# Optimization experiments

Measured on AMD Instinct MI355X. Metric: run time of the kernel, lower is better.

Reference implementation:

```python
import jax, jax.numpy as jnp
import numpy as np

DIM = 2048      # model dim
H = 32          # num_heads
N = 128         # state_dim
G = 1           # num_groups
K = 4           # conv_size
HID = 4096     # hidden_dim = multiple_of*ceil(2.0*DIM/256)
P = HID // H    # head_dim = 128
CHUNK = 256
EPS = 1e-6
DT_MIN, DT_MAX = 0.001, 0.1


def setup_inputs() -> dict:
    key = jax.random.key(0)
    ks = jax.random.split(key, 8)
    b, s = 2, 2048
    d_in = 2 * HID + 2 * G * N + H           # 8448
    conv_dim = HID + 2 * G * N               # 4352
    return {
        "x": jax.random.normal(ks[0], (b, s, DIM), jnp.float32),
        "W_in": jax.random.normal(ks[1], (d_in, DIM), jnp.float32) / np.sqrt(DIM),
        "conv_w": jax.random.normal(ks[2], (conv_dim, K), jnp.float32) / np.sqrt(K),
        "conv_b": jnp.zeros((conv_dim,), jnp.float32),
        "dt_bias": jnp.zeros((H,), jnp.float32),
        "A_log": jnp.log(jax.random.uniform(ks[3], (H,), jnp.float32, 1.0, 16.0)),
        "D": jnp.ones((H,), jnp.float32),
        "norm_w": jnp.ones((HID,), jnp.float32),
        "W_out": jax.random.normal(ks[4], (DIM, HID), jnp.float32) / np.sqrt(HID),
    }


def _causal_conv_silu(xBC, w, bias):
    # depthwise causal conv1d, kernel K, then SiLU. xBC: (b,s,c), w: (c,K)
    b, s, c = xBC.shape
    xp = jnp.pad(xBC, ((0, 0), (K - 1, 0), (0, 0)))
    y = sum(xp[:, k:k + s, :] * w[:, k] for k in range(K)) + bias
    return jax.nn.silu(y)


def _chunked_scan(x, dt, A, B, C, D):
    # Mamba2 chunked selective scan.
    # x:(b,s,h,p) dt:(b,s,h) A:(h,) B,C:(b,s,n) (groups=1) D:(h,)
    b, s, h, p = x.shape
    n = B.shape[-1]
    nc, L = s // CHUNK, CHUNK
    xc = x.reshape(b, nc, L, h, p)
    dtc = dt.reshape(b, nc, L, h)
    Bc = B.reshape(b, nc, L, n)
    Cc = C.reshape(b, nc, L, n)

    dA = dtc * A                          # (b,nc,L,h), A<0
    dA_cs = jnp.cumsum(dA, axis=2)        # (b,nc,L,h)

    # intra-chunk contribution
    seg = dA_cs[:, :, :, None, :] - dA_cs[:, :, None, :, :]   # (b,nc,L,L,h)
    mask = jnp.tril(jnp.ones((L, L), bool))[None, None, :, :, None]
    decay = jnp.exp(jnp.where(mask, seg, -jnp.inf))
    CB = jnp.einsum('bcln,bcsn->bcls', Cc, Bc)                # (b,nc,L,L)
    y_intra = jnp.einsum('bcls,bclsh,bcsh,bcshp->bclhp', CB, decay, dtc, xc)

    # per-chunk final states
    decay_states = jnp.exp(dA_cs[:, :, -1:, :] - dA_cs)       # (b,nc,L,h)
    states = jnp.einsum('bclh,bclh,bclhp,bcln->bchpn', decay_states, dtc, xc, Bc)

    # inter-chunk recurrence over chunk index
    dA_chunk = dA_cs[:, :, -1, :]                              # (b,nc,h)
    def step(prev, inp):
        st, dec = inp
        new = prev * jnp.exp(dec)[:, :, None, None] + st
        return new, prev
    init = jnp.zeros((b, h, p, n), x.dtype)
    _, prev_states = jax.lax.scan(step, init,
                                  (jnp.moveaxis(states, 1, 0), jnp.moveaxis(dA_chunk, 1, 0)))
    prev_states = jnp.moveaxis(prev_states, 0, 1)              # state at start of each chunk

    y_inter = jnp.einsum('bcln,bclh,bchpn->bclhp', Cc, jnp.exp(dA_cs), prev_states)
    y = (y_intra + y_inter).reshape(b, s, h, p)
    return y + x * D[None, None, :, None]


def reference(x, W_in, conv_w, conv_b, dt_bias, A_log, D, norm_w, W_out):
    b, s, _ = x.shape
    zxbcdt = x @ W_in.T                                        # (b,s,2*HID+2GN+H)
    z, xBC, dt = jnp.split(zxbcdt, [HID, 2 * HID + 2 * G * N], axis=-1)
    xBC = _causal_conv_silu(xBC, conv_w, conv_b)
    xs, B, C = jnp.split(xBC, [HID, HID + G * N], axis=-1)
    A = -jnp.exp(A_log)
    dt = jnp.clip(jax.nn.softplus(dt + dt_bias), DT_MIN, DT_MAX)
    xs = xs.reshape(b, s, H, P)
    y = _chunked_scan(xs, dt, A, B, C, D).reshape(b, s, HID)
    y = y * jax.nn.silu(z)                                     # gate, norm_before_gate=False
    y = y * jax.lax.rsqrt(jnp.mean(y * y, axis=-1, keepdims=True) + EPS) * norm_w
    return y @ W_out.T
```

## Files before the change

kernel.cpp:

```cpp
#include <hip/hip_runtime.h>


typedef short s16x8 __attribute__((ext_vector_type(8)));
typedef float f32x4 __attribute__((ext_vector_type(4)));

__device__ __forceinline__ float bf2f(ushort u) {
    return __builtin_bit_cast(float, (unsigned)u << 16);
}
__device__ __forceinline__ ushort f2bf(float f) {
    unsigned u = __builtin_bit_cast(unsigned, f);
    unsigned r = u + 0x7fffu + ((u >> 16) & 1u);
    return (ushort)(r >> 16);
}

__device__ __forceinline__ void gld16(const void* g, void* l) {
    __builtin_amdgcn_global_load_lds((__attribute__((address_space(1))) void*)g,
                                     (__attribute__((address_space(3))) void*)l, 16, 0, 0);
}

#define BARRIER() asm volatile("s_barrier" ::: "memory")

__global__ void cast_all_k(const float4* __restrict__ x, const float4* __restrict__ wout,
                           const float4* __restrict__ win, ushort* __restrict__ xb,
                           ushort* __restrict__ woutb, ushort* __restrict__ winb) {
    const long b = blockIdx.x, tid = threadIdx.x;
    if (b < 8192) {
        long i = b * 256 + tid;
        float4 v = x[i];
        ushort4 o = { f2bf(v.x), f2bf(v.y), f2bf(v.z), f2bf(v.w) };
        *(ushort4*)(xb + i * 4) = o;
    } else if (b < 16384) {
        long i = (b - 8192) * 256 + tid;
        float4 v = wout[i];
        ushort4 o = { f2bf(v.x), f2bf(v.y), f2bf(v.z), f2bf(v.w) };
        *(ushort4*)(woutb + i * 4) = o;
    } else {
        long i = (b - 16384) * 256 + tid;
        ushort4 o;
        if (i < 4341760L) {
            float4 v = win[i];
            o = { f2bf(v.x), f2bf(v.y), f2bf(v.z), f2bf(v.w) };
        } else {
            o = { 0, 0, 0, 0 };
        }
        *(ushort4*)(winb + i * 4) = o;
    }
}

__global__ __launch_bounds__(512, 1) void gemm1_k(const ushort* __restrict__ A,
                                                  const ushort* __restrict__ Bm,
                                                  ushort* __restrict__ zbuf,
                                                  ushort* __restrict__ xbc,
                                                  ushort* __restrict__ dtr) {
    constexpr int K = 2048, NT = 64;
    __shared__ ushort lds[3 * 8192 + 3 * 6144];
    const int tid = threadIdx.x, lane = tid & 63, wave = tid >> 6;
    const int wm = wave >> 2, wn = wave & 3;
    const int bid = blockIdx.x;
    const int xcd = bid & 7, w = bid >> 3;
    const int mt = xcd * 2 + (w & 1), nt = w >> 1;
    const long m0 = (long)mt * 256, n0 = (long)nt * 192;

    const int st_row = lane >> 2;
    const int st_gc = ((lane & 3) * 8) ^ (((lane >> 5) & 1) << 4);

    auto STAGE_A = [&](int buf, int kt) {
#pragma unroll
        for (int j = 0; j < 2; j++) {
            int sidx = wave + j * 8;
            gld16(A + (m0 + sidx * 16 + st_row) * K + kt + st_gc,
                  lds + buf * 8192 + sidx * 512 + lane * 8);
        }
    };
    auto STAGE_B = [&](int buf, int kt) {
#pragma unroll
        for (int j = 0; j < 2; j++) {
            int sidx = wave + j * 8;
            if (sidx < 12)
                gld16(Bm + (n0 + sidx * 16 + st_row) * K + kt + st_gc,
                      lds + 24576 + buf * 6144 + sidx * 512 + lane * 8);
        }
    };

    const int cfr = (lane >> 4) * 8;
    const int lr = lane & 15;
    auto LDFA = [&](int buf, int r) -> s16x8 {
        int off = buf * 8192 + ((r >> 4) << 9) + ((r & 15) << 5)
                + (cfr ^ (((r >> 3) & 1) << 4));
        return *(const s16x8*)(lds + off);
    };
    auto LDFB = [&](int buf, int r) -> s16x8 {
        int off = 24576 + buf * 6144 + ((r >> 4) << 9) + ((r & 15) << 5)
                + (cfr ^ (((r >> 3) & 1) << 4));
        return *(const s16x8*)(lds + off);
    };

    f32x4 zero = { 0.f, 0.f, 0.f, 0.f };
    f32x4 acc[8][3];
#pragma unroll
    for (int i = 0; i < 8; i++)
#pragma unroll
        for (int j = 0; j < 3; j++) acc[i][j] = zero;

    STAGE_A(0, 0);  STAGE_B(0, 0);
    STAGE_A(1, 32); STAGE_B(1, 32);
    asm volatile("s_waitcnt vmcnt(3)" ::: "memory");
    BARRIER();

    for (int t = 0; t < NT; ++t) {
        const int cur = t % 3;
        const int nxt = (t + 2) % 3;
        const int kt2 = (t + 2) * 32;
        const bool do_stage = (t + 2) < NT;

        s16x8 bfr[3], afr[4];
#pragma unroll
        for (int ni = 0; ni < 3; ni++) bfr[ni] = LDFB(cur, wn * 48 + ni * 16 + lr);
#pragma unroll
        for (int mi = 0; mi < 4; mi++) afr[mi] = LDFA(cur, wm * 128 + mi * 16 + lr);
        if (do_stage) STAGE_A(nxt, kt2);
        BARRIER();
        __builtin_amdgcn_s_setprio(1);
#pragma unroll
        for (int mi = 0; mi < 4; mi++)
#pragma unroll
            for (int ni = 0; ni < 3; ni++)
                acc[mi][ni] = __builtin_amdgcn_mfma_f32_16x16x32_bf16(afr[mi], bfr[ni], acc[mi][ni], 0, 0, 0);
        __builtin_amdgcn_s_setprio(0);
        BARRIER();

#pragma unroll
        for (int mi = 0; mi < 4; mi++) afr[mi] = LDFA(cur, wm * 128 + 64 + mi * 16 + lr);
        if (do_stage) STAGE_B(nxt, kt2);
        BARRIER();
        __builtin_amdgcn_s_setprio(1);
#pragma unroll
        for (int mi = 0; mi < 4; mi++)
#pragma unroll
            for (int ni = 0; ni < 3; ni++)
                acc[mi + 4][ni] = __builtin_amdgcn_mfma_f32_16x16x32_bf16(afr[mi], bfr[ni], acc[mi + 4][ni], 0, 0, 0);
        __builtin_amdgcn_s_setprio(0);
        asm volatile("s_waitcnt vmcnt(3)" ::: "memory");
        BARRIER();
    }

    const int lr4 = (lane >> 4) * 4;
#pragma unroll
    for (int mi = 0; mi < 8; mi++) {
#pragma unroll
        for (int ni = 0; ni < 3; ni++) {
            const long col = n0 + wn * 48 + ni * 16 + lr;
            ushort* dst;
            long stride;
            if (col < 4096)      { dst = zbuf + col;         stride = 4096; }
            else if (col < 8448) { dst = xbc + (col - 4096); stride = 4352; }
            else if (col < 8480) { dst = dtr + (col - 8448); stride = 32;   }
            else continue;
            const long row0 = m0 + wm * 128 + mi * 16 + lr4;
#pragma unroll
            for (int r = 0; r < 4; r++) dst[(row0 + r) * stride] = f2bf(acc[mi][ni][r]);
        }
    }
}

__global__ __launch_bounds__(256) void gemm_bt_k(const ushort* __restrict__ A,
                                                 const ushort* __restrict__ Bm,
                                                 float* __restrict__ Cout,
                                                 int Ncols, int Kd) {
    __shared__ ushort As[128 * 32];
    __shared__ ushort Bs[128 * 32];
    const int bid = blockIdx.x;
    const int xcd = bid & 7, w = bid >> 3;
    const int mt = xcd * 4 + (w & 3), nt = w >> 2;
    const int tid = threadIdx.x;
    const int lane = tid & 63, wave = tid >> 6;
    const int wm = wave >> 1, wn = wave & 1;
    const long m0 = (long)mt * 128, n0 = (long)nt * 128;

    f32x4 zero = { 0.f, 0.f, 0.f, 0.f };
    f32x4 acc[4][4];
#pragma unroll
    for (int i = 0; i < 4; i++)
#pragma unroll
        for (int j = 0; j < 4; j++) acc[i][j] = zero;

    const int eb = wave * 512 + lane * 8;
    for (int kt = 0; kt < Kd; kt += 32) {
        __syncthreads();
#pragma unroll
        for (int j = 0; j < 2; j++) {
            int e = j * 2048 + eb;
            int row = e >> 5, col = e & 31;
            gld16(A + (m0 + row) * Kd + kt + col, As + e);
            gld16(Bm + (n0 + row) * Kd + kt + col, Bs + e);
        }
        asm volatile("s_waitcnt vmcnt(0)" ::: "memory");
        __syncthreads();
        s16x8 af[4], bfr[4];
        const int ra = (wm * 64 + (lane & 15)) * 32 + (lane >> 4) * 8;
        const int rb = (wn * 64 + (lane & 15)) * 32 + (lane >> 4) * 8;
#pragma unroll
        for (int i = 0; i < 4; i++) {
            af[i] = *(const s16x8*)(As + ra + i * 512);
            bfr[i] = *(const s16x8*)(Bs + rb + i * 512);
        }
#pragma unroll
        for (int mi = 0; mi < 4; mi++)
#pragma unroll
            for (int ni = 0; ni < 4; ni++)
                acc[mi][ni] = __builtin_amdgcn_mfma_f32_16x16x32_bf16(af[mi], bfr[ni], acc[mi][ni], 0, 0, 0);
    }
    const long crow = m0 + wm * 64 + ((lane >> 4) << 2);
    const long ccol = n0 + wn * 64 + (lane & 15);
#pragma unroll
    for (int mi = 0; mi < 4; mi++)
#pragma unroll
        for (int ni = 0; ni < 4; ni++)
#pragma unroll
            for (int r = 0; r < 4; r++)
                Cout[(crow + mi * 16 + r) * (long)Ncols + ccol + ni * 16] = acc[mi][ni][r];
}

__global__ __launch_bounds__(256) void convx_k(const ushort* __restrict__ xbc,
                                               const float* __restrict__ w,
                                               const float* __restrict__ bias,
                                               ushort* __restrict__ xbcc,
                                               ushort* __restrict__ xT,
                                               ushort* __restrict__ Bt) {
    __shared__ ushort xin[35][136];
    __shared__ ushort yL[32][132];
    const int stile = blockIdx.x, slot = blockIdx.y, bc = blockIdx.z;
    const int tid = threadIdx.x;
    const int cc = bc & 7;
    const long tbase = (long)bc * 256 + stile * 32;
    const int c0 = slot * 128;
    const bool head = (cc == 0 && stile == 0);

#pragma unroll
    for (int i = 0; i < 3; i++) {
        int u = tid + i * 256;
        if (u < 560) {
            int r = u >> 4, seg = u & 15;
            s16x8 v;
            if (head && r < 3) {
#pragma unroll
                for (int j = 0; j < 8; j++) v[j] = 0;
            } else {
                v = *(const s16x8*)&xbc[(tbase - 3 + r) * 4352 + c0 + seg * 8];
            }
            *(s16x8*)&xin[r][seg * 8] = v;
        }
    }
    __syncthreads();

    const int s_loc = tid >> 3, p0 = (tid & 7) * 16;
    ushort yo[16];
#pragma unroll
    for (int j = 0; j < 16; j++) {
        int c = p0 + j;
        float a = bias[c0 + c];
#pragma unroll
        for (int k = 0; k < 4; k++)
            a += bf2f(xin[s_loc + k][c]) * w[(c0 + c) * 4 + k];
        float yv = a / (1.f + __expf(-a));
        ushort ub = f2bf(yv);
        yo[j] = ub;
        yL[s_loc][c] = ub;
    }
    *(s16x8*)&xbcc[(tbase + s_loc) * 4352 + c0 + p0] = *(const s16x8*)&yo[0];
    *(s16x8*)&xbcc[(tbase + s_loc) * 4352 + c0 + p0 + 8] = *(const s16x8*)&yo[8];
    __syncthreads();

    if (slot < 33) {
        const int p = tid >> 1, s0 = (tid & 1) * 16;
        ushort o[16];
#pragma unroll
        for (int j = 0; j < 16; j++) o[j] = yL[s0 + j][p];
        ushort* dst = (slot < 32)
            ? (xT + ((long)(bc * 32 + slot) * 128 + p) * 256 + stile * 32 + s0)
            : (Bt + ((long)bc * 128 + p) * 256 + stile * 32 + s0);
        *(s16x8*)&dst[0] = *(const s16x8*)&o[0];
        *(s16x8*)&dst[8] = *(const s16x8*)&o[8];
    }
}

__global__ void prep_k(const ushort* __restrict__ dtr, const float* __restrict__ dt_bias,
                       const float* __restrict__ A_log, float* __restrict__ dtp,
                       float* __restrict__ dacs) {
    const int bx = blockIdx.x;
    const int h = bx & 31, cc = (bx >> 5) & 7, bi = bx >> 8;
    const int lane = threadIdx.x;
    const float A = -__expf(A_log[h]);
    const float bsh = dt_bias[h];
    float v[4], cs[4];
    float run = 0.f;
#pragma unroll
    for (int j = 0; j < 4; j++) {
        int pos = cc * 256 + lane * 4 + j;
        float raw = bf2f(dtr[((long)(bi * 2048 + pos)) * 32 + h]) + bsh;
        float sp = (raw > 20.f) ? raw : log1pf(__expf(raw));
        float d = fminf(fmaxf(sp, 0.001f), 0.1f);
        v[j] = d;
        run += d * A;
        cs[j] = run;
    }
    float tot = run, pre = run;
    for (int off = 1; off < 64; off <<= 1) {
        float u = __shfl_up(pre, off, 64);
        if (lane >= off) pre += u;
    }
    float excl = pre - tot;
    const long base = ((long)(bi * 32 + h)) * 2048 + cc * 256 + lane * 4;
#pragma unroll
    for (int j = 0; j < 4; j++) { dtp[base + j] = v[j]; dacs[base + j] = excl + cs[j]; }
}

__global__ __launch_bounds__(256) void cb_mfma_k(const ushort* __restrict__ xbcc,
                                                 float* __restrict__ CB) {
    const int bid = blockIdx.x;
    const int sq = bid & 1, lq = (bid >> 1) & 1, bc = bid >> 2;
    const int tid = threadIdx.x, lane = tid & 63, wave = tid >> 6;
    const int wm = wave >> 1, wn = wave & 1;
    const long tbase = (long)bc * 256;

    f32x4 zero = { 0.f, 0.f, 0.f, 0.f };
    f32x4 acc[4][4];
#pragma unroll
    for (int i = 0; i < 4; i++)
#pragma unroll
        for (int j = 0; j < 4; j++) acc[i][j] = zero;

    for (int kst = 0; kst < 4; ++kst) {
        const int koff = kst * 32 + (lane >> 4) * 8;
        s16x8 a[4], b[4];
#pragma unroll
        for (int mi = 0; mi < 4; mi++) {
            int l = lq * 128 + wm * 64 + mi * 16 + (lane & 15);
            a[mi] = *(const s16x8*)&xbcc[(tbase + l) * 4352 + 4224 + koff];
        }
#pragma unroll
        for (int ni = 0; ni < 4; ni++) {
            int s = sq * 128 + wn * 64 + ni * 16 + (lane & 15);
            b[ni] = *(const s16x8*)&xbcc[(tbase + s) * 4352 + 4096 + koff];
        }
#pragma unroll
        for (int mi = 0; mi < 4; mi++)
#pragma unroll
            for (int ni = 0; ni < 4; ni++)
                acc[mi][ni] = __builtin_amdgcn_mfma_f32_16x16x32_bf16(a[mi], b[ni], acc[mi][ni], 0, 0, 0);
    }

    float* out = CB + (long)bc * 65536;
#pragma unroll
    for (int mi = 0; mi < 4; mi++)
#pragma unroll
        for (int ni = 0; ni < 4; ni++)
#pragma unroll
            for (int r = 0; r < 4; r++) {
                int l = lq * 128 + wm * 64 + mi * 16 + (lane >> 4) * 4 + r;
                int s = sq * 128 + wn * 64 + ni * 16 + (lane & 15);
                out[(long)l * 256 + s] = acc[mi][ni][r];
            }
}

__global__ __launch_bounds__(256) void intra_mfma_k(const ushort* __restrict__ xT,
                                                    const float* __restrict__ CB,
                                                    const float* __restrict__ dtp,
                                                    const float* __restrict__ dacs,
                                                    float* __restrict__ yf) {
    const int bx = blockIdx.x;
    const int ltile = bx & 1, h = (bx >> 1) & 31, cc = (bx >> 6) & 7, bi = bx >> 9;
    const int tid = threadIdx.x, lane = tid & 63, wave = tid >> 6;
    const int wm = wave >> 1, wn = wave & 1;

    __shared__ float dA_s[256];
    __shared__ float F_s[256];

    const long dbase = ((long)(bi * 32 + h)) * 2048 + cc * 256;
    {
        float a = dacs[dbase + tid];
        float r = dacs[dbase + (tid | 31)];
        dA_s[tid] = a;
        F_s[tid] = __expf(r - a) * dtp[dbase + tid];
    }
    __syncthreads();

    int lch[4];
    float dAl[4];
#pragma unroll
    for (int mi = 0; mi < 4; mi++) {
        lch[mi] = ltile * 128 + wm * 64 + mi * 16 + (lane & 15);
        dAl[mi] = dA_s[lch[mi]];
    }

    f32x4 zero = { 0.f, 0.f, 0.f, 0.f };
    f32x4 acc[4][4];
#pragma unroll
    for (int i = 0; i < 4; i++)
#pragma unroll
        for (int j = 0; j < 4; j++) acc[i][j] = zero;

    const long tbase = (long)bi * 2048 + cc * 256;
    const long cbbase = ((long)(bi * 8 + cc)) * 65536;
    const ushort* xrow = xT + (((long)(bi * 8 + cc) * 32 + h) * 128) * 256;
    const int nsb = ltile * 4 + 4;

    for (int sb = 0; sb < nsb; ++sb) {
        const int soff = sb * 32 + (lane >> 4) * 8;
        s16x8 bf[4];
#pragma unroll
        for (int ni = 0; ni < 4; ni++) {
            int p = wn * 64 + ni * 16 + (lane & 15);
            bf[ni] = *(const s16x8*)&xrow[(long)p * 256 + soff];
        }
        const float Rsb = dA_s[sb * 32 + 31];
        const int s0 = soff;
#pragma unroll
        for (int mi = 0; mi < 4; mi++) {
            const int lb = lch[mi] >> 5;
            if (sb > lb) continue;
            const float* cbrow = CB + cbbase + (long)lch[mi] * 256 + s0;
            float4 c0 = *(const float4*)cbrow;
            float4 c1 = *(const float4*)(cbrow + 4);
            float E = __expf(dAl[mi] - Rsb);
            float m[8];
            m[0] = c0.x * E * F_s[s0 + 0]; m[1] = c0.y * E * F_s[s0 + 1];
            m[2] = c0.z * E * F_s[s0 + 2]; m[3] = c0.w * E * F_s[s0 + 3];
            m[4] = c1.x * E * F_s[s0 + 4]; m[5] = c1.y * E * F_s[s0 + 5];
            m[6] = c1.z * E * F_s[s0 + 6]; m[7] = c1.w * E * F_s[s0 + 7];
            if (sb == lb) {
#pragma unroll
                for (int j = 0; j < 8; j++)
                    if (s0 + j > lch[mi]) m[j] = 0.f;
            }
            s16x8 a;
#pragma unroll
            for (int j = 0; j < 8; j++) a[j] = (short)f2bf(m[j]);
#pragma unroll
            for (int ni = 0; ni < 4; ni++)
                acc[mi][ni] = __builtin_amdgcn_mfma_f32_16x16x32_bf16(a, bf[ni], acc[mi][ni], 0, 0, 0);
        }
    }

    const long crow = tbase + ltile * 128 + wm * 64 + ((lane >> 4) << 2);
    const int ccol = h * 128 + wn * 64 + (lane & 15);
#pragma unroll
    for (int mi = 0; mi < 4; mi++)
#pragma unroll
        for (int ni = 0; ni < 4; ni++)
#pragma unroll
            for (int r = 0; r < 4; r++)
                yf[(crow + mi * 16 + r) * 4096 + ccol + ni * 16] = acc[mi][ni][r];
}

__global__ __launch_bounds__(256) void states_mfma_k(const ushort* __restrict__ xT,
                                                     const ushort* __restrict__ Bt,
                                                     const float* __restrict__ dtp,
                                                     const float* __restrict__ dacs,
                                                     float* __restrict__ states) {
    const int bx = blockIdx.x;
    const int h = bx & 31, cc = (bx >> 5) & 7, bi = bx >> 8;
    const int bc = bi * 8 + cc;
    const int tid = threadIdx.x, lane = tid & 63, wave = tid >> 6;
    const int wm = wave >> 1, wn = wave & 1;
    __shared__ float wl[256];
    const long dbase = ((long)(bi * 32 + h)) * 2048 + cc * 256;
    {
        float last = dacs[dbase + 255];
        wl[tid] = __expf(last - dacs[dbase + tid]) * dtp[dbase + tid];
    }
    __syncthreads();

    f32x4 zero = { 0.f, 0.f, 0.f, 0.f };
    f32x4 acc[4][4];
#pragma unroll
    for (int i = 0; i < 4; i++)
#pragma unroll
        for (int j = 0; j < 4; j++) acc[i][j] = zero;

    const ushort* xrow = xT + (((long)bc * 32 + h) * 128) * 256;
    const ushort* brow = Bt + ((long)bc * 128) * 256;

    for (int sb = 0; sb < 8; ++sb) {
        const int soff = sb * 32 + (lane >> 4) * 8;
        s16x8 a[4], b[4];
#pragma unroll
        for (int mi = 0; mi < 4; mi++) {
            int p = wm * 64 + mi * 16 + (lane & 15);
            s16x8 raw = *(const s16x8*)&xrow[(long)p * 256 + soff];
#pragma unroll
            for (int j = 0; j < 8; j++)
                a[mi][j] = (short)f2bf(bf2f((ushort)raw[j]) * wl[soff + j]);
        }
#pragma unroll
        for (int ni = 0; ni < 4; ni++) {
            int n = wn * 64 + ni * 16 + (lane & 15);
            b[ni] = *(const s16x8*)&brow[(long)n * 256 + soff];
        }
#pragma unroll
        for (int mi = 0; mi < 4; mi++)
#pragma unroll
            for (int ni = 0; ni < 4; ni++)
                acc[mi][ni] = __builtin_amdgcn_mfma_f32_16x16x32_bf16(a[mi], b[ni], acc[mi][ni], 0, 0, 0);
    }

    float* out = states + (((long)bc * 32 + h) * 128) * 128;
#pragma unroll
    for (int mi = 0; mi < 4; mi++)
#pragma unroll
        for (int ni = 0; ni < 4; ni++)
#pragma unroll
            for (int r = 0; r < 4; r++) {
                int p = wm * 64 + mi * 16 + (lane >> 4) * 4 + r;
                int n = wn * 64 + ni * 16 + (lane & 15);
                out[(long)p * 128 + n] = acc[mi][ni][r];
            }
}

__global__ void rec_k(float* __restrict__ states, const float* __restrict__ dacs) {
    const int i = blockIdx.x * 256 + threadIdx.x;
    const int n = i & 127, p = (i >> 7) & 127, h = (i >> 14) & 31, bi = i >> 19;
    const long dbase = ((long)(bi * 32 + h)) * 2048;
    float run = 0.f;
    for (int cc = 0; cc < 8; cc++) {
        const long off = ((((long)(bi * 8 + cc)) * 32 + h) * 128 + p) * 128 + n;
        float st = states[off];
        states[off] = run;
        float dec = dacs[dbase + cc * 256 + 255];
        run = run * __expf(dec) + st;
    }
}

__global__ __launch_bounds__(256) void inter_mfma_k(const ushort* __restrict__ xbcc,
                                                    const float* __restrict__ st,
                                                    const float* __restrict__ dacs,
                                                    float* __restrict__ yf) {
    const int bx = blockIdx.x;
    const int lt = bx & 1, h = (bx >> 1) & 31, cc = (bx >> 6) & 7, bi = bx >> 9;
    const int tid = threadIdx.x, lane = tid & 63, wave = tid >> 6;
    const int wm = wave >> 1, wn = wave & 1;
    __shared__ float eA[256];
    const long dbase = ((long)(bi * 32 + h)) * 2048 + cc * 256;
    eA[tid] = __expf(dacs[dbase + tid]);
    __syncthreads();

    const long tbase = (long)bi * 2048 + cc * 256;
    const float* sbase = st + (((long)(bi * 8 + cc) * 32 + h) * 128) * 128;

    f32x4 zero = { 0.f, 0.f, 0.f, 0.f };
    f32x4 acc[4][4];
#pragma unroll
    for (int i = 0; i < 4; i++)
#pragma unroll
        for (int j = 0; j < 4; j++) acc[i][j] = zero;

    for (int kk = 0; kk < 4; ++kk) {
        const int koff = kk * 32 + (lane >> 4) * 8;
        s16x8 a[4], b[4];
#pragma unroll
        for (int mi = 0; mi < 4; mi++) {
            int l = lt * 128 + wm * 64 + mi * 16 + (lane & 15);
            a[mi] = *(const s16x8*)&xbcc[(tbase + l) * 4352 + 4224 + koff];
        }
#pragma unroll
        for (int ni = 0; ni < 4; ni++) {
            int p = wn * 64 + ni * 16 + (lane & 15);
            const float* pr = sbase + (long)p * 128 + koff;
            float4 v0 = *(const float4*)pr;
            float4 v1 = *(const float4*)(pr + 4);
            b[ni][0] = (short)f2bf(v0.x); b[ni][1] = (short)f2bf(v0.y);
            b[ni][2] = (short)f2bf(v0.z); b[ni][3] = (short)f2bf(v0.w);
            b[ni][4] = (short)f2bf(v1.x); b[ni][5] = (short)f2bf(v1.y);
            b[ni][6] = (short)f2bf(v1.z); b[ni][7] = (short)f2bf(v1.w);
        }
#pragma unroll
        for (int mi = 0; mi < 4; mi++)
#pragma unroll
            for (int ni = 0; ni < 4; ni++)
                acc[mi][ni] = __builtin_amdgcn_mfma_f32_16x16x32_bf16(a[mi], b[ni], acc[mi][ni], 0, 0, 0);
    }

#pragma unroll
    for (int mi = 0; mi < 4; mi++)
#pragma unroll
        for (int r = 0; r < 4; r++) {
            int l = lt * 128 + wm * 64 + mi * 16 + (lane >> 4) * 4 + r;
            float e = eA[l];
            float* yr = &yf[(tbase + l) * 4096 + h * 128];
#pragma unroll
            for (int ni = 0; ni < 4; ni++) {
                int p = wn * 64 + ni * 16 + (lane & 15);
                yr[p] += e * acc[mi][ni][r];
            }
        }
}

__global__ __launch_bounds__(256) void gate_rms_k(const float* __restrict__ y, const ushort* __restrict__ zbuf,
                                                  const ushort* __restrict__ xbcc, const float* __restrict__ Dv,
                                                  const float* __restrict__ norm_w, ushort* __restrict__ yb) {
    const int t = blockIdx.x, tid = threadIdx.x;
    const float* yr = &y[(long)t * 4096];
    const ushort* zr = &zbuf[(long)t * 4096];
    const ushort* xr = &xbcc[(long)t * 4352];
    float g[16];
    float ss = 0.f;
#pragma unroll
    for (int j = 0; j < 16; j++) {
        int i = j * 256 + tid;
        float z = bf2f(zr[i]);
        float yv = yr[i] + Dv[i >> 7] * bf2f(xr[i]);
        float gv = yv * (z / (1.f + __expf(-z)));
        g[j] = gv;
        ss += gv * gv;
    }
#pragma unroll
    for (int off = 32; off > 0; off >>= 1) ss += __shfl_xor(ss, off, 64);
    __shared__ float red[4];
    if ((tid & 63) == 0) red[tid >> 6] = ss;
    __syncthreads();
    float tot = red[0] + red[1] + red[2] + red[3];
    float sc = rsqrtf(tot * (1.f / 4096.f) + 1e-6f);
#pragma unroll
    for (int j = 0; j < 16; j++) {
        int i = j * 256 + tid;
        yb[(long)t * 4096 + i] = f2bf(g[j] * sc * norm_w[i]);
    }
}

extern "C" void kernel_launch(void* const* d_in, const int* in_sizes, int n_in,
                              void* d_out, int out_size, void* d_ws, size_t ws_size,
                              hipStream_t stream) {
    const float* x       = (const float*)d_in[0];
    const float* W_in    = (const float*)d_in[1];
    const float* conv_w  = (const float*)d_in[2];
    const float* conv_b  = (const float*)d_in[3];
    const float* dt_bias = (const float*)d_in[4];
    const float* A_log   = (const float*)d_in[5];
    const float* Dv      = (const float*)d_in[6];
    const float* norm_w  = (const float*)d_in[7];
    const float* W_out   = (const float*)d_in[8];

    char* w8 = (char*)d_ws;
    ushort* xb    = (ushort*)(w8 + 0L);
    ushort* xT    = (ushort*)(w8 + 0L);
    ushort* yb    = (ushort*)(w8 + 0L);
    ushort* woutb = (ushort*)(w8 + 33554432L);
    ushort* Bt    = (ushort*)(w8 + 50331648L);
    ushort* zbuf  = (ushort*)(w8 + 52428800L);
    ushort* xbc   = (ushort*)(w8 + 85983232L);
    ushort* dtr   = (ushort*)(w8 + 121634816L);
    ushort* xbcc  = (ushort*)(w8 + 121896960L);
    float*  dtp   = (float*)(w8 + 157548544L);
    float*  dacs  = (float*)(w8 + 158072832L);
    float*  cb    = (float*)(w8 + 158597120L);
    float*  yf    = (float*)(w8 + 162791424L);
    ushort* winb  = (ushort*)(w8 + 162791424L);
    float*  st    = (float*)(w8 + 229900288L);

    cast_all_k<<<34048, 256, 0, stream>>>((const float4*)x, (const float4*)W_out,
                                          (const float4*)W_in, xb, woutb, winb);
    gemm1_k<<<736, 512, 0, stream>>>(xb, winb, zbuf, xbc, dtr);
    convx_k<<<dim3(8, 34, 16), 256, 0, stream>>>(xbc, conv_w, conv_b, xbcc, xT, Bt);
    prep_k<<<512, 64, 0, stream>>>(dtr, dt_bias, A_log, dtp, dacs);
    cb_mfma_k<<<64, 256, 0, stream>>>(xbcc, cb);
    intra_mfma_k<<<1024, 256, 0, stream>>>(xT, cb, dtp, dacs, yf);
    states_mfma_k<<<512, 256, 0, stream>>>(xT, Bt, dtp, dacs, st);
    rec_k<<<4096, 256, 0, stream>>>(st, dacs);
    inter_mfma_k<<<1024, 256, 0, stream>>>(xbcc, st, dacs, yf);
    gate_rms_k<<<4096, 256, 0, stream>>>(yf, zbuf, xbcc, Dv, norm_w, yb);
    gemm_bt_k<<<512, 256, 0, stream>>>(yb, woutb, (float*)d_out, 2048, 4096);
}
```

Measured before the change: 502.3 us.

## Fuse intra and inter chunk scan kernels; pipeline output GEMM with triple buffering

The intra-chunk and inter-chunk kernels are merged into one scan kernel. It adds the C·state contribution, with C pre-scaled by exp(dA_cs), into the same accumulators before the single write of yf. This removes one kernel launch and a read-modify-write pass over the fp32 y buffer. The output projection GEMM is replaced by a 256x128-tile, 512-thread kernel with a three-stage LDS pipeline, XOR-swizzled LDS layout and setprio around the MFMAs, aiming to overlap loads with compute. The C pre-scaling rounds to bf16 after multiplying, which slightly changes numerics.

```diff
diff --git a/kernel.cpp b/kernel.cpp
--- a/kernel.cpp
+++ b/kernel.cpp
@@ -163,62 +163,109 @@
     }
 }
 
-__global__ __launch_bounds__(256) void gemm_bt_k(const ushort* __restrict__ A,
-                                                 const ushort* __restrict__ Bm,
-                                                 float* __restrict__ Cout,
-                                                 int Ncols, int Kd) {
-    __shared__ ushort As[128 * 32];
-    __shared__ ushort Bs[128 * 32];
+__global__ __launch_bounds__(512, 1) void gemm2_k(const ushort* __restrict__ A,
+                                                  const ushort* __restrict__ Bm,
+                                                  float* __restrict__ Cout) {
+    constexpr int K = 4096, NT = 128;
+    __shared__ ushort lds[3 * 8192 + 3 * 4096];
+    const int tid = threadIdx.x, lane = tid & 63, wave = tid >> 6;
+    const int wm = wave >> 2, wn = wave & 3;
     const int bid = blockIdx.x;
     const int xcd = bid & 7, w = bid >> 3;
-    const int mt = xcd * 4 + (w & 3), nt = w >> 2;
-    const int tid = threadIdx.x;
-    const int lane = tid & 63, wave = tid >> 6;
-    const int wm = wave >> 1, wn = wave & 1;
-    const long m0 = (long)mt * 128, n0 = (long)nt * 128;
+    const int mt = xcd * 2 + (w & 1), nt = w >> 1;
+    const long m0 = (long)mt * 256, n0 = (long)nt * 128;
+
+    const int st_row = lane >> 2;
+    const int st_gc = ((lane & 3) * 8) ^ (((lane >> 5) & 1) << 4);
+
+    auto STAGE_A = [&](int buf, int kt) {
+#pragma unroll
+        for (int j = 0; j < 2; j++) {
+            int sidx = wave + j * 8;
+            gld16(A + (m0 + sidx * 16 + st_row) * K + kt + st_gc,
+                  lds + buf * 8192 + sidx * 512 + lane * 8);
+        }
+    };
+    auto STAGE_B = [&](int buf, int kt) {
+        int sidx = wave;
+        gld16(Bm + (n0 + sidx * 16 + st_row) * K + kt + st_gc,
+              lds + 24576 + buf * 4096 + sidx * 512 + lane * 8);
+    };
+
+    const int cfr = (lane >> 4) * 8;
+    const int lr = lane & 15;
+    auto LDFA = [&](int buf, int r) -> s16x8 {
+        int off = buf * 8192 + ((r >> 4) << 9) + ((r & 15) << 5)
+                + (cfr ^ (((r >> 3) & 1) << 4));
+        return *(const s16x8*)(lds + off);
+    };
+    auto LDFB = [&](int buf, int r) -> s16x8 {
+        int off = 24576 + buf * 4096 + ((r >> 4) << 9) + ((r & 15) << 5)
+                + (cfr ^ (((r >> 3) & 1) << 4));
+        return *(const s16x8*)(lds + off);
+    };
 
     f32x4 zero = { 0.f, 0.f, 0.f, 0.f };
-    f32x4 acc[4][4];
-#pragma unroll
-    for (int i = 0; i < 4; i++)
-#pragma unroll
-        for (int j = 0; j < 4; j++) acc[i][j] = zero;
-
-    const int eb = wave * 512 + lane * 8;
-    for (int kt = 0; kt < Kd; kt += 32) {
-        __syncthreads();
-#pragma unroll
-        for (int j = 0; j < 2; j++) {
-            int e = j * 2048 + eb;
-            int row = e >> 5, col = e & 31;
-            gld16(A + (m0 + row) * Kd + kt + col, As + e);
-            gld16(Bm + (n0 + row) * Kd + kt + col, Bs + e);
-        }
-        asm volatile("s_waitcnt vmcnt(0)" ::: "memory");
-        __syncthreads();
-        s16x8 af[4], bfr[4];
-        const int ra = (wm * 64 + (lane & 15)) * 32 + (lane >> 4) * 8;
-        const int rb = (wn * 64 + (lane & 15)) * 32 + (lane >> 4) * 8;
-#pragma unroll
-        for (int i = 0; i < 4; i++) {
-            af[i] = *(const s16x8*)(As + ra + i * 512);
-            bfr[i] = *(const s16x8*)(Bs + rb + i * 512);
-        }
+    f32x4 acc[8][2];
+#pragma unroll
+    for (int i = 0; i < 8; i++)
+#pragma unroll
+        for (int j = 0; j < 2; j++) acc[i][j] = zero;
+
+    STAGE_A(0, 0);  STAGE_B(0, 0);
+    STAGE_A(1, 32); STAGE_B(1, 32);
+    asm volatile("s_waitcnt vmcnt(2)" ::: "memory");
+    BARRIER();
+
+    for (int t = 0; t < NT; ++t) {
+        const int cur = t % 3;
+        const int nxt = (t + 2) % 3;
+        const int kt2 = (t + 2) * 32;
+        const bool do_stage = (t + 2) < NT;
+
+        s16x8 bfr[2], afr[4];
+#pragma unroll
+        for (int ni = 0; ni < 2; ni++) bfr[ni] = LDFB(cur, wn * 32 + ni * 16 + lr);
+#pragma unroll
+        for (int mi = 0; mi < 4; mi++) afr[mi] = LDFA(cur, wm * 128 + mi * 16 + lr);
+        if (do_stage) STAGE_A(nxt, kt2);
+        BARRIER();
+        __builtin_amdgcn_s_setprio(1);
 #pragma unroll
         for (int mi = 0; mi < 4; mi++)
 #pragma unroll
-            for (int ni = 0; ni < 4; ni++)
-                acc[mi][ni] = __builtin_amdgcn_mfma_f32_16x16x32_bf16(af[mi], bfr[ni], acc[mi][ni], 0, 0, 0);
-    }
-    const long crow = m0 + wm * 64 + ((lane >> 4) << 2);
-    const long ccol = n0 + wn * 64 + (lane & 15);
-#pragma unroll
-    for (int mi = 0; mi < 4; mi++)
-#pragma unroll
-        for (int ni = 0; ni < 4; ni++)
+            for (int ni = 0; ni < 2; ni++)
+                acc[mi][ni] = __builtin_amdgcn_mfma_f32_16x16x32_bf16(afr[mi], bfr[ni], acc[mi][ni], 0, 0, 0);
+        __builtin_amdgcn_s_setprio(0);
+        BARRIER();
+
+#pragma unroll
+        for (int mi = 0; mi < 4; mi++) afr[mi] = LDFA(cur, wm * 128 + 64 + mi * 16 + lr);
+        if (do_stage) STAGE_B(nxt, kt2);
+        BARRIER();
+        __builtin_amdgcn_s_setprio(1);
+#pragma unroll
+        for (int mi = 0; mi < 4; mi++)
+#pragma unroll
+            for (int ni = 0; ni < 2; ni++)
+                acc[mi + 4][ni] = __builtin_amdgcn_mfma_f32_16x16x32_bf16(afr[mi], bfr[ni], acc[mi + 4][ni], 0, 0, 0);
+        __builtin_amdgcn_s_setprio(0);
+        asm volatile("s_waitcnt vmcnt(2)" ::: "memory");
+        BARRIER();
+    }
+
+    const int lr4 = (lane >> 4) * 4;
+#pragma unroll
+    for (int mi = 0; mi < 8; mi++) {
+#pragma unroll
+        for (int ni = 0; ni < 2; ni++) {
+            const long col = n0 + wn * 32 + ni * 16 + lr;
+            const long row0 = m0 + wm * 128 + mi * 16 + lr4;
 #pragma unroll
             for (int r = 0; r < 4; r++)
-                Cout[(crow + mi * 16 + r) * (long)Ncols + ccol + ni * 16] = acc[mi][ni][r];
+                Cout[(row0 + r) * 2048 + col] = acc[mi][ni][r];
+        }
+    }
 }
 
 __global__ __launch_bounds__(256) void convx_k(const ushort* __restrict__ xbc,
@@ -363,11 +410,13 @@
             }
 }
 
-__global__ __launch_bounds__(256) void intra_mfma_k(const ushort* __restrict__ xT,
-                                                    const float* __restrict__ CB,
-                                                    const float* __restrict__ dtp,
-                                                    const float* __restrict__ dacs,
-                                                    float* __restrict__ yf) {
+__global__ __launch_bounds__(256) void scan_mfma_k(const ushort* __restrict__ xT,
+                                                   const float* __restrict__ CB,
+                                                   const float* __restrict__ dtp,
+                                                   const float* __restrict__ dacs,
+                                                   const ushort* __restrict__ xbcc,
+                                                   const float* __restrict__ st,
+                                                   float* __restrict__ yf) {
     const int bx = blockIdx.x;
     const int ltile = bx & 1, h = (bx >> 1) & 31, cc = (bx >> 6) & 7, bi = bx >> 9;
     const int tid = threadIdx.x, lane = tid & 63, wave = tid >> 6;
@@ -440,6 +489,38 @@
             for (int ni = 0; ni < 4; ni++)
                 acc[mi][ni] = __builtin_amdgcn_mfma_f32_16x16x32_bf16(a, bf[ni], acc[mi][ni], 0, 0, 0);
         }
+    }
+
+    const float* sbase = st + (((long)(bi * 8 + cc) * 32 + h) * 128) * 128;
+    float eAr[4];
+#pragma unroll
+    for (int mi = 0; mi < 4; mi++) eAr[mi] = __expf(dAl[mi]);
+    for (int kk = 0; kk < 4; ++kk) {
+        const int koff = kk * 32 + (lane >> 4) * 8;
+        s16x8 a[4], b[4];
+#pragma unroll
+        for (int mi = 0; mi < 4; mi++) {
+            s16x8 raw = *(const s16x8*)&xbcc[(tbase + lch[mi]) * 4352 + 4224 + koff];
+#pragma unroll
+            for (int j = 0; j < 8; j++)
+                a[mi][j] = (short)f2bf(bf2f((ushort)raw[j]) * eAr[mi]);
+        }
+#pragma unroll
+        for (int ni = 0; ni < 4; ni++) {
+            int p = wn * 64 + ni * 16 + (lane & 15);
+            const float* pr = sbase + (long)p * 128 + koff;
+            float4 v0 = *(const float4*)pr;
+            float4 v1 = *(const float4*)(pr + 4);
+            b[ni][0] = (short)f2bf(v0.x); b[ni][1] = (short)f2bf(v0.y);
+            b[ni][2] = (short)f2bf(v0.z); b[ni][3] = (short)f2bf(v0.w);
+            b[ni][4] = (short)f2bf(v1.x); b[ni][5] = (short)f2bf(v1.y);
+            b[ni][6] = (short)f2bf(v1.z); b[ni][7] = (short)f2bf(v1.w);
+        }
+#pragma unroll
+        for (int mi = 0; mi < 4; mi++)
+#pragma unroll
+            for (int ni = 0; ni < 4; ni++)
+                acc[mi][ni] = __builtin_amdgcn_mfma_f32_16x16x32_bf16(a[mi], b[ni], acc[mi][ni], 0, 0, 0);
     }
 
     const long crow = tbase + ltile * 128 + wm * 64 + ((lane >> 4) << 2);
@@ -529,70 +610,6 @@
         float dec = dacs[dbase + cc * 256 + 255];
         run = run * __expf(dec) + st;
     }
-}
-
-__global__ __launch_bounds__(256) void inter_mfma_k(const ushort* __restrict__ xbcc,
-                                                    const float* __restrict__ st,
-                                                    const float* __restrict__ dacs,
-                                                    float* __restrict__ yf) {
-    const int bx = blockIdx.x;
-    const int lt = bx & 1, h = (bx >> 1) & 31, cc = (bx >> 6) & 7, bi = bx >> 9;
-    const int tid = threadIdx.x, lane = tid & 63, wave = tid >> 6;
-    const int wm = wave >> 1, wn = wave & 1;
-    __shared__ float eA[256];
-    const long dbase = ((long)(bi * 32 + h)) * 2048 + cc * 256;
-    eA[tid] = __expf(dacs[dbase + tid]);
-    __syncthreads();
-
-    const long tbase = (long)bi * 2048 + cc * 256;
-    const float* sbase = st + (((long)(bi * 8 + cc) * 32 + h) * 128) * 128;
-
-    f32x4 zero = { 0.f, 0.f, 0.f, 0.f };
-    f32x4 acc[4][4];
-#pragma unroll
-    for (int i = 0; i < 4; i++)
-#pragma unroll
-        for (int j = 0; j < 4; j++) acc[i][j] = zero;
-
-    for (int kk = 0; kk < 4; ++kk) {
-        const int koff = kk * 32 + (lane >> 4) * 8;
-        s16x8 a[4], b[4];
-#pragma unroll
-        for (int mi = 0; mi < 4; mi++) {
-            int l = lt * 128 + wm * 64 + mi * 16 + (lane & 15);
-            a[mi] = *(const s16x8*)&xbcc[(tbase + l) * 4352 + 4224 + koff];
-        }
-#pragma unroll
-        for (int ni = 0; ni < 4; ni++) {
-            int p = wn * 64 + ni * 16 + (lane & 15);
-            const float* pr = sbase + (long)p * 128 + koff;
-            float4 v0 = *(const float4*)pr;
-            float4 v1 = *(const float4*)(pr + 4);
-            b[ni][0] = (short)f2bf(v0.x); b[ni][1] = (short)f2bf(v0.y);
-            b[ni][2] = (short)f2bf(v0.z); b[ni][3] = (short)f2bf(v0.w);
-            b[ni][4] = (short)f2bf(v1.x); b[ni][5] = (short)f2bf(v1.y);
-            b[ni][6] = (short)f2bf(v1.z); b[ni][7] = (short)f2bf(v1.w);
-        }
-#pragma unroll
-        for (int mi = 0; mi < 4; mi++)
-#pragma unroll
-            for (int ni = 0; ni < 4; ni++)
-                acc[mi][ni] = __builtin_amdgcn_mfma_f32_16x16x32_bf16(a[mi], b[ni], acc[mi][ni], 0, 0, 0);
-    }
-
-#pragma unroll
-    for (int mi = 0; mi < 4; mi++)
-#pragma unroll
-        for (int r = 0; r < 4; r++) {
-            int l = lt * 128 + wm * 64 + mi * 16 + (lane >> 4) * 4 + r;
-            float e = eA[l];
-            float* yr = &yf[(tbase + l) * 4096 + h * 128];
-#pragma unroll
-            for (int ni = 0; ni < 4; ni++) {
-                int p = wn * 64 + ni * 16 + (lane & 15);
-                yr[p] += e * acc[mi][ni][r];
-            }
-        }
 }
 
 __global__ __launch_bounds__(256) void gate_rms_k(const float* __restrict__ y, const ushort* __restrict__ zbuf,
@@ -663,10 +680,9 @@
     convx_k<<<dim3(8, 34, 16), 256, 0, stream>>>(xbc, conv_w, conv_b, xbcc, xT, Bt);
     prep_k<<<512, 64, 0, stream>>>(dtr, dt_bias, A_log, dtp, dacs);
     cb_mfma_k<<<64, 256, 0, stream>>>(xbcc, cb);
-    intra_mfma_k<<<1024, 256, 0, stream>>>(xT, cb, dtp, dacs, yf);
     states_mfma_k<<<512, 256, 0, stream>>>(xT, Bt, dtp, dacs, st);
     rec_k<<<4096, 256, 0, stream>>>(st, dacs);
-    inter_mfma_k<<<1024, 256, 0, stream>>>(xbcc, st, dacs, yf);
+    scan_mfma_k<<<1024, 256, 0, stream>>>(xT, cb, dtp, dacs, xbcc, st, yf);
     gate_rms_k<<<4096, 256, 0, stream>>>(yf, zbuf, xbcc, Dv, norm_w, yb);
-    gemm_bt_k<<<512, 256, 0, stream>>>(yb, woutb, (float*)d_out, 2048, 4096);
-}
+    gemm2_k<<<256, 512, 0, stream>>>(yb, woutb, (float*)d_out);
+}
```

Measured after the change: 464.0 us. 1.08x faster.
